# Performance work log

Hardware: AMD Instinct MI355X
Metric: run time of the kernel (lower is better)

Reference implementation:

```python
import jax, jax.numpy as jnp
import numpy as np

B, D, K, U = 4096, 1024, 5, 1024  # batch, input_dim, num_basis, units


def setup_inputs() -> dict:
    key = jax.random.key(0)
    k1, k2, k3 = jax.random.split(key, 3)
    x = jax.random.normal(k1, (B, D), dtype=jnp.float32)
    basis_weights = jax.random.normal(k2, (D, K, U), dtype=jnp.float32) * 0.02
    bias = jax.random.normal(k3, (U,), dtype=jnp.float32) * 0.02
    return {"x": x, "basis_weights": basis_weights, "bias": bias}


def reference(x, basis_weights, bias):
    # Polynomial basis expansion: x^0, x^1, ..., x^{K-1}  -> (B, D, K)
    num_basis = basis_weights.shape[1]
    powers = jnp.arange(num_basis, dtype=x.dtype)
    basis = x[..., None] ** powers  # x**0 == 1, matching tf.ones_like branch
    # Fused: einsum('bik,ikj->bij') followed by reduce_sum over i == 'bik,ikj->bj'.
    # Avoids materializing the (B, D, U) intermediate of the original.
    out = jnp.einsum("bik,ikj->bj", basis, basis_weights) + bias
    # tf.nn.gelu defaults to exact (non-approximate) GELU.
    return jax.nn.gelu(out, approximate=False)
```

## Files before the change

### kernel.cpp

```cpp
#include <hip/hip_runtime.h>
#include <hip/hip_bf16.h>
#include <math.h>


#define B_DIM 4096
#define D_DIM 1024
#define U_DIM 1024
#define KT2 4096
#define NKB 128

typedef unsigned short ushort_t;
typedef __attribute__((ext_vector_type(8))) short bf16x8;
typedef __attribute__((ext_vector_type(4))) float f32x4;

__device__ __forceinline__ ushort_t f2bf(float f) {
  union { float f; unsigned int u; } v;
  v.f = f;
  unsigned int r = v.u + 0x7FFFu + ((v.u >> 16) & 1u);
  return (ushort_t)(r >> 16);
}

__device__ __forceinline__ void load_lds16(const ushort_t* g, ushort_t* l) {
  __builtin_amdgcn_global_load_lds(
      (const __attribute__((address_space(1))) ushort_t*)g,
      (__attribute__((address_space(3))) ushort_t*)l, 16, 0, 0);
}

__device__ __forceinline__ float gelu_exact(float v) {
  return 0.5f * v * (1.0f + erff(v * 0.70710678118654752f));
}


__global__ __launch_bounds__(256) void basis_pack_kernel(
    const float* __restrict__ x, ushort_t* __restrict__ Ap) {
  const int t    = threadIdx.x;
  const int wave = t >> 6;
  const int lane = t & 63;
  const int kblk = blockIdx.x * 4 + wave;
  const int m16  = blockIdx.y;
  const int m    = lane & 15;
  const int ko   = lane >> 4;
  const int row  = m16 * 16 + m;
  const int i0   = kblk * 8 + ko * 2;

  const float xa = x[(size_t)row * D_DIM + i0];
  const float xb = x[(size_t)row * D_DIM + i0 + 1];
  const float xa2 = xa * xa, xb2 = xb * xb;
  ushort_t o[8];
  o[0] = f2bf(xa);  o[1] = f2bf(xa2); o[2] = f2bf(xa2 * xa); o[3] = f2bf(xa2 * xa2);
  o[4] = f2bf(xb);  o[5] = f2bf(xb2); o[6] = f2bf(xb2 * xb); o[7] = f2bf(xb2 * xb2);
  *(uint4*)(Ap + ((size_t)m16 * NKB + kblk) * 512 + lane * 8) = *(const uint4*)o;
}

__global__ __launch_bounds__(256) void w_pack_kernel(
    const float* __restrict__ W, ushort_t* __restrict__ Bp) {
  const int t    = threadIdx.x;
  const int wave = t >> 6;
  const int lane = t & 63;
  const int kblk = blockIdx.x * 4 + wave;
  const int n16  = blockIdx.y;
  const int jj   = lane & 15;
  const int ko   = lane >> 4;
  const int j    = n16 * 16 + jj;
  const int i0   = kblk * 8 + ko * 2;

  ushort_t o[8];
#pragma unroll
  for (int t2 = 0; t2 < 2; ++t2) {
    const int i = i0 + t2;
#pragma unroll
    for (int e = 0; e < 4; ++e) {
      const int r = i * 5 + e + 1;
      o[t2 * 4 + e] = f2bf(W[(size_t)r * U_DIM + j]);
    }
  }
  *(uint4*)(Bp + ((size_t)n16 * NKB + kblk) * 512 + lane * 8) = *(const uint4*)o;
}

__global__ __launch_bounds__(256) void fold_part_kernel(
    const float* __restrict__ W, float* __restrict__ part) {
  const int j = blockIdx.x * 256 + threadIdx.x;
  const int g = blockIdx.y;
  float s = 0.0f;
#pragma unroll 8
  for (int ii = 0; ii < 32; ++ii) {
    const int i = g * 32 + ii;
    s += W[(size_t)(i * 5) * U_DIM + j];
  }
  part[(size_t)g * U_DIM + j] = s;
}

__global__ __launch_bounds__(256) void fold_final_kernel(
    const float* __restrict__ part, const float* __restrict__ bias,
    float* __restrict__ bias2) {
  const int j = blockIdx.x * 256 + threadIdx.x;
  float s = bias[j];
#pragma unroll
  for (int g = 0; g < 32; ++g) s += part[(size_t)g * U_DIM + j];
  bias2[j] = s;
}

__global__ __launch_bounds__(256) void gemm_kernel(
    const ushort_t* __restrict__ Ap, const ushort_t* __restrict__ Bp,
    const float* __restrict__ bias2, float* __restrict__ C) {
  __shared__ ushort_t lds[4][12 * 512];

  const int tid  = threadIdx.x;
  const int wave = tid >> 6;
  const int lane = tid & 63;
  const int wm   = wave >> 1;
  const int wn   = wave & 1;
  const int m16b = blockIdx.y * 4;
  const int n16b = blockIdx.x * 8;

  const ushort_t* gsrc[3];
  int ldst[3];
#pragma unroll
  for (int s = 0; s < 3; ++s) {
    const int u = s * 4 + wave;
    const ushort_t* base = (u < 4)
        ? Ap + ((size_t)(m16b + u) * NKB) * 512
        : Bp + ((size_t)(n16b + (u - 4)) * NKB) * 512;
    gsrc[s] = base + lane * 8;
    ldst[s] = u * 512 + lane * 8;
  }

  f32x4 acc[2][4];
  const f32x4 zero = {0.0f, 0.0f, 0.0f, 0.0f};
#pragma unroll
  for (int mf = 0; mf < 2; ++mf)
#pragma unroll
    for (int nf = 0; nf < 4; ++nf) acc[mf][nf] = zero;

#define STAGE(bb, it)                                                   \
  do {                                                                  \
    _Pragma("unroll")                                                   \
    for (int s = 0; s < 3; ++s)                                         \
      load_lds16(gsrc[s] + (size_t)(it) * 512, &lds[bb][ldst[s]]);      \
  } while (0)

#define COMPUTE(bb)                                                     \
  do {                                                                  \
    bf16x8 a[2], b[4];                                                  \
    _Pragma("unroll")                                                   \
    for (int mf = 0; mf < 2; ++mf)                                      \
      a[mf] = *(const bf16x8*)&lds[bb][(wm * 2 + mf) * 512 + lane * 8]; \
    _Pragma("unroll")                                                   \
    for (int nf = 0; nf < 4; ++nf)                                      \
      b[nf] = *(const bf16x8*)&lds[bb][(4 + wn * 4 + nf) * 512 + lane * 8]; \
    _Pragma("unroll")                                                   \
    for (int mf = 0; mf < 2; ++mf)                                      \
      _Pragma("unroll")                                                 \
      for (int nf = 0; nf < 4; ++nf)                                    \
        acc[mf][nf] = __builtin_amdgcn_mfma_f32_16x16x32_bf16(          \
            a[mf], b[nf], acc[mf][nf], 0, 0, 0);                        \
  } while (0)

  STAGE(0, 0);
  STAGE(1, 1);
  STAGE(2, 2);

  for (int it = 0; it < 125; ++it) {
    asm volatile("s_waitcnt vmcnt(6)\n\ts_barrier" ::: "memory");
    STAGE((it + 3) & 3, it + 3);
    COMPUTE(it & 3);
  }
  asm volatile("s_waitcnt vmcnt(6)\n\ts_barrier" ::: "memory");
  COMPUTE(1);
  asm volatile("s_waitcnt vmcnt(3)\n\ts_barrier" ::: "memory");
  COMPUTE(2);
  asm volatile("s_waitcnt vmcnt(0)\n\ts_barrier" ::: "memory");
  COMPUTE(3);
#undef STAGE
#undef COMPUTE

  const int crow0 = m16b * 16 + wm * 32 + (lane >> 4) * 4;
  const int ccol0 = n16b * 16 + wn * 64 + (lane & 15);
#pragma unroll
  for (int nf = 0; nf < 4; ++nf) {
    const int col = ccol0 + nf * 16;
    const float bv = bias2[col];
#pragma unroll
    for (int mf = 0; mf < 2; ++mf) {
#pragma unroll
      for (int r = 0; r < 4; ++r) {
        const int row = crow0 + mf * 16 + r;
        C[(size_t)row * U_DIM + col] = gelu_exact(acc[mf][nf][r] + bv);
      }
    }
  }
}

__global__ void fallback_kernel(const float* __restrict__ x, const float* __restrict__ W,
                                const float* __restrict__ bias, float* __restrict__ out) {
  int j  = blockIdx.x * 256 + threadIdx.x;
  int b0 = blockIdx.y * 16;
  float acc[16];
#pragma unroll
  for (int t = 0; t < 16; ++t) acc[t] = 0.0f;
  for (int i = 0; i < D_DIM; ++i) {
    const float* wr = W + (size_t)i * 5 * U_DIM + j;
    float w0 = wr[0 * U_DIM], w1 = wr[1 * U_DIM], w2 = wr[2 * U_DIM];
    float w3 = wr[3 * U_DIM], w4 = wr[4 * U_DIM];
#pragma unroll
    for (int t = 0; t < 16; ++t) {
      float xv = x[(size_t)(b0 + t) * D_DIM + i];
      float x2 = xv * xv;
      acc[t] += w0 + xv * w1 + x2 * w2 + x2 * xv * w3 + x2 * x2 * w4;
    }
  }
  float bv = bias[j];
#pragma unroll
  for (int t = 0; t < 16; ++t)
    out[(size_t)(b0 + t) * U_DIM + j] = gelu_exact(acc[t] + bv);
}

extern "C" void kernel_launch(void* const* d_in, const int* in_sizes, int n_in,
                              void* d_out, int out_size, void* d_ws, size_t ws_size,
                              hipStream_t stream) {
  const float* x    = (const float*)d_in[0];
  const float* W    = (const float*)d_in[1];
  const float* bias = (const float*)d_in[2];
  float* out = (float*)d_out;

  const size_t szA = (size_t)B_DIM * KT2 * sizeof(ushort_t);
  const size_t szB = (size_t)U_DIM * KT2 * sizeof(ushort_t);
  const size_t szP = (size_t)32 * U_DIM * sizeof(float);
  const size_t szb = (size_t)U_DIM * sizeof(float);

  if (ws_size >= szA + szB + szP + szb) {
    ushort_t* Ap   = (ushort_t*)d_ws;
    ushort_t* Bp   = (ushort_t*)((char*)d_ws + szA);
    float*    part = (float*)((char*)d_ws + szA + szB);
    float*    b2   = (float*)((char*)d_ws + szA + szB + szP);
    basis_pack_kernel<<<dim3(NKB / 4, B_DIM / 16), 256, 0, stream>>>(x, Ap);
    w_pack_kernel<<<dim3(NKB / 4, U_DIM / 16), 256, 0, stream>>>(W, Bp);
    fold_part_kernel<<<dim3(U_DIM / 256, 32), 256, 0, stream>>>(W, part);
    fold_final_kernel<<<dim3(U_DIM / 256), 256, 0, stream>>>(part, bias, b2);
    gemm_kernel<<<dim3(U_DIM / 128, B_DIM / 64), 256, 0, stream>>>(Ap, Bp, b2, out);
  } else {
    fallback_kernel<<<dim3(U_DIM / 256, B_DIM / 16), 256, 0, stream>>>(x, W, bias, out);
  }
}
```

Before: 152.2 us.

## Fuse basis expansion into GEMM and fold bias sum into weight packing

Removes the separate basis_pack pass: the GEMM now loads raw x, computes the powers, converts them to bf16 and writes the A tiles into LDS inside a 5-buffer software pipeline, which avoids writing and re-reading a 32 MB packed A buffer. The x^0 weight row sum is now accumulated in w_pack via shuffles and atomics into a bias buffer initialised by a tiny kernel, replacing the two fold kernels. The block index is also remapped so that consecutive blocks on the same XCD share B tiles. The cost is VALU work and more LDS inside the GEMM loop, plus float atomics that make the bias sum order nondeterministic.

```diff
diff --git a/kernel.cpp b/kernel.cpp
--- a/kernel.cpp
+++ b/kernel.cpp
@@ -12,6 +12,7 @@
 typedef unsigned short ushort_t;
 typedef __attribute__((ext_vector_type(8))) short bf16x8;
 typedef __attribute__((ext_vector_type(4))) float f32x4;
+typedef __attribute__((ext_vector_type(2))) float f32x2;
 
 __device__ __forceinline__ ushort_t f2bf(float f) {
   union { float f; unsigned int u; } v;
@@ -31,29 +32,15 @@
 }
 
 
-__global__ __launch_bounds__(256) void basis_pack_kernel(
-    const float* __restrict__ x, ushort_t* __restrict__ Ap) {
-  const int t    = threadIdx.x;
-  const int wave = t >> 6;
-  const int lane = t & 63;
-  const int kblk = blockIdx.x * 4 + wave;
-  const int m16  = blockIdx.y;
-  const int m    = lane & 15;
-  const int ko   = lane >> 4;
-  const int row  = m16 * 16 + m;
-  const int i0   = kblk * 8 + ko * 2;
-
-  const float xa = x[(size_t)row * D_DIM + i0];
-  const float xb = x[(size_t)row * D_DIM + i0 + 1];
-  const float xa2 = xa * xa, xb2 = xb * xb;
-  ushort_t o[8];
-  o[0] = f2bf(xa);  o[1] = f2bf(xa2); o[2] = f2bf(xa2 * xa); o[3] = f2bf(xa2 * xa2);
-  o[4] = f2bf(xb);  o[5] = f2bf(xb2); o[6] = f2bf(xb2 * xb); o[7] = f2bf(xb2 * xb2);
-  *(uint4*)(Ap + ((size_t)m16 * NKB + kblk) * 512 + lane * 8) = *(const uint4*)o;
+__global__ __launch_bounds__(256) void init_b2_kernel(
+    const float* __restrict__ bias, float* __restrict__ b2) {
+  const int j = blockIdx.x * 256 + threadIdx.x;
+  b2[j] = bias[j];
 }
 
 __global__ __launch_bounds__(256) void w_pack_kernel(
-    const float* __restrict__ W, ushort_t* __restrict__ Bp) {
+    const float* __restrict__ W, ushort_t* __restrict__ Bp,
+    float* __restrict__ b2) {
   const int t    = threadIdx.x;
   const int wave = t >> 6;
   const int lane = t & 63;
@@ -65,9 +52,11 @@
   const int i0   = kblk * 8 + ko * 2;
 
   ushort_t o[8];
+  float s0 = 0.0f;
 #pragma unroll
   for (int t2 = 0; t2 < 2; ++t2) {
     const int i = i0 + t2;
+    s0 += W[(size_t)(i * 5) * U_DIM + j];
 #pragma unroll
     for (int e = 0; e < 4; ++e) {
       const int r = i * 5 + e + 1;
@@ -75,55 +64,44 @@
     }
   }
   *(uint4*)(Bp + ((size_t)n16 * NKB + kblk) * 512 + lane * 8) = *(const uint4*)o;
-}
-
-__global__ __launch_bounds__(256) void fold_part_kernel(
-    const float* __restrict__ W, float* __restrict__ part) {
-  const int j = blockIdx.x * 256 + threadIdx.x;
-  const int g = blockIdx.y;
-  float s = 0.0f;
-#pragma unroll 8
-  for (int ii = 0; ii < 32; ++ii) {
-    const int i = g * 32 + ii;
-    s += W[(size_t)(i * 5) * U_DIM + j];
-  }
-  part[(size_t)g * U_DIM + j] = s;
-}
-
-__global__ __launch_bounds__(256) void fold_final_kernel(
-    const float* __restrict__ part, const float* __restrict__ bias,
-    float* __restrict__ bias2) {
-  const int j = blockIdx.x * 256 + threadIdx.x;
-  float s = bias[j];
-#pragma unroll
-  for (int g = 0; g < 32; ++g) s += part[(size_t)g * U_DIM + j];
-  bias2[j] = s;
+  s0 += __shfl_xor(s0, 16, 64);
+  s0 += __shfl_xor(s0, 32, 64);
+  if (ko == 0) atomicAdd(&b2[j], s0);
 }
 
 __global__ __launch_bounds__(256) void gemm_kernel(
-    const ushort_t* __restrict__ Ap, const ushort_t* __restrict__ Bp,
-    const float* __restrict__ bias2, float* __restrict__ C) {
-  __shared__ ushort_t lds[4][12 * 512];
+    const float* __restrict__ x, const ushort_t* __restrict__ Bp,
+    const float* __restrict__ b2, float* __restrict__ C) {
+  __shared__ __align__(16) ushort_t lds[5][12 * 512];
 
   const int tid  = threadIdx.x;
   const int wave = tid >> 6;
   const int lane = tid & 63;
   const int wm   = wave >> 1;
   const int wn   = wave & 1;
-  const int m16b = blockIdx.y * 4;
-  const int n16b = blockIdx.x * 8;
-
-  const ushort_t* gsrc[3];
-  int ldst[3];
-#pragma unroll
-  for (int s = 0; s < 3; ++s) {
-    const int u = s * 4 + wave;
-    const ushort_t* base = (u < 4)
-        ? Ap + ((size_t)(m16b + u) * NKB) * 512
-        : Bp + ((size_t)(n16b + (u - 4)) * NKB) * 512;
-    gsrc[s] = base + lane * 8;
-    ldst[s] = u * 512 + lane * 8;
-  }
+
+  const int lin  = blockIdx.y * 8 + blockIdx.x;
+  const int xcd  = lin & 7;
+  const int slot = lin >> 3;
+  const int mt   = xcd * 8 + (slot & 7);
+  const int nt   = slot >> 3;
+  const int m16b = mt * 4;
+  const int n16b = nt * 8;
+
+  const ushort_t* gsrcB[2];
+  int ldstB[2];
+#pragma unroll
+  for (int s = 0; s < 2; ++s) {
+    const int u = 4 + s * 4 + wave;
+    gsrcB[s] = Bp + ((size_t)(n16b + (u - 4)) * NKB) * 512 + lane * 8;
+    ldstB[s] = u * 512 + lane * 8;
+  }
+
+  const int m     = lane & 15;
+  const int ko    = lane >> 4;
+  const int arow  = (m16b + wave) * 16 + m;
+  const float* xsrc = x + (size_t)arow * D_DIM + ko * 2;
+  const int ldstA = wave * 512 + lane * 8;
 
   f32x4 acc[2][4];
   const f32x4 zero = {0.0f, 0.0f, 0.0f, 0.0f};
@@ -132,11 +110,30 @@
 #pragma unroll
     for (int nf = 0; nf < 4; ++nf) acc[mf][nf] = zero;
 
-#define STAGE(bb, it)                                                   \
+  f32x2 xr[4];
+
+#define FENCE asm volatile("" ::: "memory")
+#define WAITBAR(N) \
+  asm volatile("s_waitcnt vmcnt(" #N ") lgkmcnt(0)\n\ts_barrier" ::: "memory")
+
+#define STAGE_B(bb, it)                                                 \
   do {                                                                  \
-    _Pragma("unroll")                                                   \
-    for (int s = 0; s < 3; ++s)                                         \
-      load_lds16(gsrc[s] + (size_t)(it) * 512, &lds[bb][ldst[s]]);      \
+    load_lds16(gsrcB[0] + (size_t)(it) * 512, &lds[bb][ldstB[0]]);      \
+    load_lds16(gsrcB[1] + (size_t)(it) * 512, &lds[bb][ldstB[1]]);      \
+  } while (0)
+
+#define LOADX(sl, it) xr[sl] = *(const f32x2*)(xsrc + (size_t)(it) * 8)
+
+#define WRITEA(bb, sl)                                                  \
+  do {                                                                  \
+    const float xa = xr[sl][0], xb = xr[sl][1];                         \
+    const float xa2 = xa * xa, xb2 = xb * xb;                           \
+    ushort_t o[8];                                                      \
+    o[0] = f2bf(xa);  o[1] = f2bf(xa2);                                 \
+    o[2] = f2bf(xa2 * xa); o[3] = f2bf(xa2 * xa2);                      \
+    o[4] = f2bf(xb);  o[5] = f2bf(xb2);                                 \
+    o[6] = f2bf(xb2 * xb); o[7] = f2bf(xb2 * xb2);                      \
+    *(uint4*)(&lds[bb][ldstA]) = *(const uint4*)o;                      \
   } while (0)
 
 #define COMPUTE(bb)                                                     \
@@ -156,30 +153,89 @@
             a[mf], b[nf], acc[mf][nf], 0, 0, 0);                        \
   } while (0)
 
-  STAGE(0, 0);
-  STAGE(1, 1);
-  STAGE(2, 2);
-
-  for (int it = 0; it < 125; ++it) {
-    asm volatile("s_waitcnt vmcnt(6)\n\ts_barrier" ::: "memory");
-    STAGE((it + 3) & 3, it + 3);
-    COMPUTE(it & 3);
-  }
-  asm volatile("s_waitcnt vmcnt(6)\n\ts_barrier" ::: "memory");
+  LOADX(0, 0);
+  LOADX(1, 1);
+  asm volatile("s_waitcnt vmcnt(0)" ::: "memory");
+  WRITEA(0, 0);
+  WRITEA(1, 1);
+  FENCE;
+  LOADX(2, 2); FENCE;
+  STAGE_B(0, 0); FENCE;
+  LOADX(3, 3); FENCE;
+  STAGE_B(1, 1); FENCE;
+  LOADX(0, 4); FENCE;
+  STAGE_B(2, 2);
+  STAGE_B(3, 3);
+
+  int bc = 0, ba = 2, bs = 4;
+  for (int base = 0; base < 120; base += 4) {
+#pragma unroll
+    for (int j = 0; j < 4; ++j) {
+      const int it = base + j;
+      WAITBAR(8);
+      LOADX((j + 1) & 3, it + 5);
+      FENCE;
+      STAGE_B(bs, it + 4);
+      FENCE;
+      WRITEA(ba, (j + 2) & 3);
+      COMPUTE(bc);
+      bc = (bc == 4) ? 0 : bc + 1;
+      ba = (ba == 4) ? 0 : ba + 1;
+      bs = (bs == 4) ? 0 : bs + 1;
+    }
+  }
+
+  WAITBAR(8);
+  LOADX(1, 125); FENCE;
+  STAGE_B(4, 124); FENCE;
+  WRITEA(2, 2);
+  COMPUTE(0);
+
+  WAITBAR(8);
+  LOADX(2, 126); FENCE;
+  STAGE_B(0, 125); FENCE;
+  WRITEA(3, 3);
   COMPUTE(1);
-  asm volatile("s_waitcnt vmcnt(3)\n\ts_barrier" ::: "memory");
+
+  WAITBAR(8);
+  LOADX(3, 127); FENCE;
+  STAGE_B(1, 126); FENCE;
+  WRITEA(4, 0);
   COMPUTE(2);
-  asm volatile("s_waitcnt vmcnt(0)\n\ts_barrier" ::: "memory");
+
+  WAITBAR(8);
+  STAGE_B(2, 127);
+  FENCE;
+  WRITEA(0, 1);
   COMPUTE(3);
-#undef STAGE
+
+  WAITBAR(7);
+  WRITEA(1, 2);
+  COMPUTE(4);
+
+  WAITBAR(4);
+  WRITEA(2, 3);
+  COMPUTE(0);
+
+  WAITBAR(2);
+  COMPUTE(1);
+
+  WAITBAR(0);
+  COMPUTE(2);
+
+#undef STAGE_B
+#undef LOADX
+#undef WRITEA
 #undef COMPUTE
+#undef WAITBAR
+#undef FENCE
 
   const int crow0 = m16b * 16 + wm * 32 + (lane >> 4) * 4;
   const int ccol0 = n16b * 16 + wn * 64 + (lane & 15);
 #pragma unroll
   for (int nf = 0; nf < 4; ++nf) {
     const int col = ccol0 + nf * 16;
-    const float bv = bias2[col];
+    const float bv = b2[col];
 #pragma unroll
     for (int mf = 0; mf < 2; ++mf) {
 #pragma unroll
@@ -223,21 +279,15 @@
   const float* bias = (const float*)d_in[2];
   float* out = (float*)d_out;
 
-  const size_t szA = (size_t)B_DIM * KT2 * sizeof(ushort_t);
   const size_t szB = (size_t)U_DIM * KT2 * sizeof(ushort_t);
-  const size_t szP = (size_t)32 * U_DIM * sizeof(float);
   const size_t szb = (size_t)U_DIM * sizeof(float);
 
-  if (ws_size >= szA + szB + szP + szb) {
-    ushort_t* Ap   = (ushort_t*)d_ws;
-    ushort_t* Bp   = (ushort_t*)((char*)d_ws + szA);
-    float*    part = (float*)((char*)d_ws + szA + szB);
-    float*    b2   = (float*)((char*)d_ws + szA + szB + szP);
-    basis_pack_kernel<<<dim3(NKB / 4, B_DIM / 16), 256, 0, stream>>>(x, Ap);
-    w_pack_kernel<<<dim3(NKB / 4, U_DIM / 16), 256, 0, stream>>>(W, Bp);
-    fold_part_kernel<<<dim3(U_DIM / 256, 32), 256, 0, stream>>>(W, part);
-    fold_final_kernel<<<dim3(U_DIM / 256), 256, 0, stream>>>(part, bias, b2);
-    gemm_kernel<<<dim3(U_DIM / 128, B_DIM / 64), 256, 0, stream>>>(Ap, Bp, b2, out);
+  if (ws_size >= szB + szb) {
+    ushort_t* Bp = (ushort_t*)d_ws;
+    float*    b2 = (float*)((char*)d_ws + szB);
+    init_b2_kernel<<<dim3(U_DIM / 256), 256, 0, stream>>>(bias, b2);
+    w_pack_kernel<<<dim3(NKB / 4, U_DIM / 16), 256, 0, stream>>>(W, Bp, b2);
+    gemm_kernel<<<dim3(U_DIM / 128, B_DIM / 64), 256, 0, stream>>>(x, Bp, b2, out);
   } else {
     fallback_kernel<<<dim3(U_DIM / 256, B_DIM / 16), 256, 0, stream>>>(x, W, bias, out);
   }
```

Result: slower. 162.7 us (+6.9%).

## Fuse bias fold into weight pack via atomics, swizzle GEMM tiles per XCD

Applied to the files above, without the earlier changes.

Removes the two separate fold kernels. The x^0 weight row sum is now computed inside w_pack_kernel with wave shuffles and atomicAdd, and the accumulator is zeroed in basis_pack_kernel, which cuts two launches and the partial buffer. The GEMM block index is remapped so that neighbouring M tiles land on the same XCD, aiming for better L2 reuse of A and B. The main loop is also unrolled by 4 with constant LDS buffer indices and pointer bumps. Float atomics make the bias sum order nondeterministic, and the zeroing relies on the basis kernel finishing before the w_pack atomics run, which stream ordering guarantees.

```diff
diff --git a/kernel.cpp b/kernel.cpp
--- a/kernel.cpp
+++ b/kernel.cpp
@@ -32,7 +32,12 @@
 
 
 __global__ __launch_bounds__(256) void basis_pack_kernel(
-    const float* __restrict__ x, ushort_t* __restrict__ Ap) {
+    const float* __restrict__ x, ushort_t* __restrict__ Ap,
+    float* __restrict__ fold) {
+  if (blockIdx.x == 0 && blockIdx.y == 0) {
+#pragma unroll
+    for (int q = 0; q < 4; ++q) fold[q * 256 + threadIdx.x] = 0.0f;
+  }
   const int t    = threadIdx.x;
   const int wave = t >> 6;
   const int lane = t & 63;
@@ -53,7 +58,8 @@
 }
 
 __global__ __launch_bounds__(256) void w_pack_kernel(
-    const float* __restrict__ W, ushort_t* __restrict__ Bp) {
+    const float* __restrict__ W, ushort_t* __restrict__ Bp,
+    float* __restrict__ fold) {
   const int t    = threadIdx.x;
   const int wave = t >> 6;
   const int lane = t & 63;
@@ -65,9 +71,11 @@
   const int i0   = kblk * 8 + ko * 2;
 
   ushort_t o[8];
+  float s0 = 0.0f;
 #pragma unroll
   for (int t2 = 0; t2 < 2; ++t2) {
     const int i = i0 + t2;
+    s0 += W[(size_t)(i * 5) * U_DIM + j];
 #pragma unroll
     for (int e = 0; e < 4; ++e) {
       const int r = i * 5 + e + 1;
@@ -75,45 +83,32 @@
     }
   }
   *(uint4*)(Bp + ((size_t)n16 * NKB + kblk) * 512 + lane * 8) = *(const uint4*)o;
-}
-
-__global__ __launch_bounds__(256) void fold_part_kernel(
-    const float* __restrict__ W, float* __restrict__ part) {
-  const int j = blockIdx.x * 256 + threadIdx.x;
-  const int g = blockIdx.y;
-  float s = 0.0f;
-#pragma unroll 8
-  for (int ii = 0; ii < 32; ++ii) {
-    const int i = g * 32 + ii;
-    s += W[(size_t)(i * 5) * U_DIM + j];
-  }
-  part[(size_t)g * U_DIM + j] = s;
-}
-
-__global__ __launch_bounds__(256) void fold_final_kernel(
-    const float* __restrict__ part, const float* __restrict__ bias,
-    float* __restrict__ bias2) {
-  const int j = blockIdx.x * 256 + threadIdx.x;
-  float s = bias[j];
-#pragma unroll
-  for (int g = 0; g < 32; ++g) s += part[(size_t)g * U_DIM + j];
-  bias2[j] = s;
+  s0 += __shfl_xor(s0, 16, 64);
+  s0 += __shfl_xor(s0, 32, 64);
+  if (ko == 0) atomicAdd(&fold[j], s0);
 }
 
 __global__ __launch_bounds__(256) void gemm_kernel(
     const ushort_t* __restrict__ Ap, const ushort_t* __restrict__ Bp,
-    const float* __restrict__ bias2, float* __restrict__ C) {
-  __shared__ ushort_t lds[4][12 * 512];
+    const float* __restrict__ bias, const float* __restrict__ fold,
+    float* __restrict__ C) {
+  __shared__ __align__(16) ushort_t lds[4][12 * 512];
 
   const int tid  = threadIdx.x;
   const int wave = tid >> 6;
   const int lane = tid & 63;
   const int wm   = wave >> 1;
   const int wn   = wave & 1;
-  const int m16b = blockIdx.y * 4;
-  const int n16b = blockIdx.x * 8;
-
-  const ushort_t* gsrc[3];
+
+  const int lin  = blockIdx.y * 8 + blockIdx.x;
+  const int xcd  = lin & 7;
+  const int slot = lin >> 3;
+  const int mt   = xcd * 8 + (slot & 7);
+  const int nt   = slot >> 3;
+  const int m16b = mt * 4;
+  const int n16b = nt * 8;
+
+  const ushort_t* gcur[3];
   int ldst[3];
 #pragma unroll
   for (int s = 0; s < 3; ++s) {
@@ -121,7 +116,7 @@
     const ushort_t* base = (u < 4)
         ? Ap + ((size_t)(m16b + u) * NKB) * 512
         : Bp + ((size_t)(n16b + (u - 4)) * NKB) * 512;
-    gsrc[s] = base + lane * 8;
+    gcur[s] = base + lane * 8;
     ldst[s] = u * 512 + lane * 8;
   }
 
@@ -132,11 +127,14 @@
 #pragma unroll
     for (int nf = 0; nf < 4; ++nf) acc[mf][nf] = zero;
 
-#define STAGE(bb, it)                                                   \
+#define WAITBAR(N) \
+  asm volatile("s_waitcnt vmcnt(" #N ")\n\ts_barrier" ::: "memory")
+
+#define STAGE_REL(bb, rel)                                              \
   do {                                                                  \
     _Pragma("unroll")                                                   \
     for (int s = 0; s < 3; ++s)                                         \
-      load_lds16(gsrc[s] + (size_t)(it) * 512, &lds[bb][ldst[s]]);      \
+      load_lds16(gcur[s] + (rel) * 512, &lds[bb][ldst[s]]);             \
   } while (0)
 
 #define COMPUTE(bb)                                                     \
@@ -156,30 +154,34 @@
             a[mf], b[nf], acc[mf][nf], 0, 0, 0);                        \
   } while (0)
 
-  STAGE(0, 0);
-  STAGE(1, 1);
-  STAGE(2, 2);
-
-  for (int it = 0; it < 125; ++it) {
-    asm volatile("s_waitcnt vmcnt(6)\n\ts_barrier" ::: "memory");
-    STAGE((it + 3) & 3, it + 3);
-    COMPUTE(it & 3);
-  }
-  asm volatile("s_waitcnt vmcnt(6)\n\ts_barrier" ::: "memory");
-  COMPUTE(1);
-  asm volatile("s_waitcnt vmcnt(3)\n\ts_barrier" ::: "memory");
-  COMPUTE(2);
-  asm volatile("s_waitcnt vmcnt(0)\n\ts_barrier" ::: "memory");
-  COMPUTE(3);
-#undef STAGE
+  STAGE_REL(0, 0);
+  STAGE_REL(1, 1);
+  STAGE_REL(2, 2);
+#pragma unroll
+  for (int s = 0; s < 3; ++s) gcur[s] += 4 * 512;
+
+  for (int base = 0; base < 124; base += 4) {
+    WAITBAR(6); STAGE_REL(3, -1); COMPUTE(0);
+    WAITBAR(6); STAGE_REL(0,  0); COMPUTE(1);
+    WAITBAR(6); STAGE_REL(1,  1); COMPUTE(2);
+    WAITBAR(6); STAGE_REL(2,  2); COMPUTE(3);
+#pragma unroll
+    for (int s = 0; s < 3; ++s) gcur[s] += 4 * 512;
+  }
+  WAITBAR(6); STAGE_REL(3, -1); COMPUTE(0);
+  WAITBAR(6); COMPUTE(1);
+  WAITBAR(3); COMPUTE(2);
+  WAITBAR(0); COMPUTE(3);
+#undef STAGE_REL
 #undef COMPUTE
+#undef WAITBAR
 
   const int crow0 = m16b * 16 + wm * 32 + (lane >> 4) * 4;
   const int ccol0 = n16b * 16 + wn * 64 + (lane & 15);
 #pragma unroll
   for (int nf = 0; nf < 4; ++nf) {
     const int col = ccol0 + nf * 16;
-    const float bv = bias2[col];
+    const float bv = bias[col] + fold[col];
 #pragma unroll
     for (int mf = 0; mf < 2; ++mf) {
 #pragma unroll
@@ -225,19 +227,15 @@
 
   const size_t szA = (size_t)B_DIM * KT2 * sizeof(ushort_t);
   const size_t szB = (size_t)U_DIM * KT2 * sizeof(ushort_t);
-  const size_t szP = (size_t)32 * U_DIM * sizeof(float);
-  const size_t szb = (size_t)U_DIM * sizeof(float);
-
-  if (ws_size >= szA + szB + szP + szb) {
+  const size_t szF = (size_t)U_DIM * sizeof(float);
+
+  if (ws_size >= szA + szB + szF) {
     ushort_t* Ap   = (ushort_t*)d_ws;
     ushort_t* Bp   = (ushort_t*)((char*)d_ws + szA);
-    float*    part = (float*)((char*)d_ws + szA + szB);
-    float*    b2   = (float*)((char*)d_ws + szA + szB + szP);
-    basis_pack_kernel<<<dim3(NKB / 4, B_DIM / 16), 256, 0, stream>>>(x, Ap);
-    w_pack_kernel<<<dim3(NKB / 4, U_DIM / 16), 256, 0, stream>>>(W, Bp);
-    fold_part_kernel<<<dim3(U_DIM / 256, 32), 256, 0, stream>>>(W, part);
-    fold_final_kernel<<<dim3(U_DIM / 256), 256, 0, stream>>>(part, bias, b2);
-    gemm_kernel<<<dim3(U_DIM / 128, B_DIM / 64), 256, 0, stream>>>(Ap, Bp, b2, out);
+    float*    fld  = (float*)((char*)d_ws + szA + szB);
+    basis_pack_kernel<<<dim3(NKB / 4, B_DIM / 16), 256, 0, stream>>>(x, Ap, fld);
+    w_pack_kernel<<<dim3(NKB / 4, U_DIM / 16), 256, 0, stream>>>(W, Bp, fld);
+    gemm_kernel<<<dim3(U_DIM / 128, B_DIM / 64), 256, 0, stream>>>(Ap, Bp, bias, fld, out);
   } else {
     fallback_kernel<<<dim3(U_DIM / 256, B_DIM / 16), 256, 0, stream>>>(x, W, bias, out);
   }
```

Result: faster. 137.1 us (-9.9%).
